# Kernel tuning notes

Hardware: AMD Instinct MI355X
Metric: run time of the kernel (lower is better)

Reference implementation:

```python
import jax, jax.numpy as jnp
import numpy as np

BN_EPS = 1e-5

def _bn(x, g, b):
    # BatchNorm1d, training-mode batch statistics
    mu = x.mean(axis=0)
    var = x.var(axis=0)
    return g * (x - mu) / jnp.sqrt(var + BN_EPS) + b

def setup_inputs() -> dict:
    key = jax.random.key(0)
    ks = jax.random.split(key, 10)
    B2, D_in, D1, DIMS, C = 16384, 1024, 512, 256, 40
    B = B2 // 2
    def w(k, shape, fan_in):
        return jax.random.normal(k, shape, jnp.float32) / np.float32(np.sqrt(fan_in))
    return {
        "lufeat": jax.random.normal(ks[0], (B2, D_in), jnp.float32),
        "llabel": jax.random.randint(ks[1], (B,), 0, C),
        "W1": w(ks[2], (D_in, D1), D_in), "b1": jnp.zeros(D1, jnp.float32),
        "W2": w(ks[3], (D1, DIMS), D1), "b2": jnp.zeros(DIMS, jnp.float32),
        "W3": w(ks[4], (DIMS + C, 256), DIMS + C), "b3": jnp.zeros(256, jnp.float32),
        "W4": w(ks[5], (256, 64), 256), "b4": jnp.zeros(64, jnp.float32),
        "W5": w(ks[6], (64, 1), 64), "b5": jnp.zeros(1, jnp.float32),
        "g1": jnp.ones(256, jnp.float32), "be1": jnp.zeros(256, jnp.float32),
        "g2": jnp.ones(64, jnp.float32), "be2": jnp.zeros(64, jnp.float32),
        "mbank0": jax.random.normal(ks[7], (C, DIMS), jnp.float32),
        "start0": jnp.zeros(C, jnp.float32),
    }

def reference(lufeat, llabel, W1, b1, W2, b2, W3, b3, W4, b4, W5, b5,
              g1, be1, g2, be2, mbank0, start0):
    B = lufeat.shape[0] // 2
    h = (lufeat @ W1 + b1) @ W2 + b2            # [2B, dims]
    h = h / jnp.linalg.norm(h, axis=1, keepdims=True)
    lfeat, ufeat = h[:B], h[B:]

    # Sequential per-sample memory-bank scatter/EMA update (detached feats)
    lf_sg = jax.lax.stop_gradient(lfeat)
    def step(carry, xs):
        start, mbank = carry
        lab, feat = xs
        row = jnp.where(start[lab] == 0, feat, 0.9 * mbank[lab] + 0.1 * feat)
        return (start.at[lab].set(1.0), mbank.at[lab].set(row)), None
    (_, mbank), _ = jax.lax.scan(step, (start0, mbank0), (llabel, lf_sg))
    mbank = jax.lax.stop_gradient(mbank)

    # cdist retrieval: [B, C] euclidean distances
    lm = jnp.linalg.norm(lfeat[:, None, :] - mbank[None, :, :], axis=-1)
    lscores = lm.min(axis=-1)
    um = jnp.linalg.norm(ufeat[:, None, :] - mbank[None, :, :], axis=-1)

    uf = jnp.concatenate([ufeat, um], axis=-1)   # [B, dims + C]
    u = jax.nn.relu(_bn(uf @ W3 + b3, g1, be1))
    u = jax.nn.relu(_bn(u @ W4 + b4, g2, be2))   # dropout = identity (eval)
    uscores = u @ W5 + b5                        # [B, 1]
    return lscores, uscores, mbank
```

## Files before the change

### kernel.cpp

```cpp
#include <hip/hip_runtime.h>
#include <hip/hip_bf16.h>
#include <stdint.h>

typedef __attribute__((ext_vector_type(4))) float f32x4;
typedef __attribute__((ext_vector_type(8))) short s16x8;
typedef __attribute__((ext_vector_type(4))) unsigned short u16x4;
typedef __attribute__((ext_vector_type(4))) int i32x4;

#define B2T 16384
#define BH 8192
#define DIN 1024
#define DD1 512
#define DIMS 256
#define NC 40
#define CAPS 2048

__device__ __forceinline__ unsigned short f2b(float f) {
  unsigned int u = __builtin_bit_cast(unsigned int, f);
  u += 0x7FFFu + ((u >> 16) & 1u);
  return (unsigned short)(u >> 16);
}

__device__ __forceinline__ float b2f(unsigned short u) {
  return __builtin_bit_cast(float, ((unsigned int)u) << 16);
}

__device__ __forceinline__ void gload16(const void* g, void* l) {
  __builtin_amdgcn_global_load_lds(
      (const __attribute__((address_space(1))) void*)g,
      (__attribute__((address_space(3))) void*)l, 16, 0, 0);
}

__global__ __launch_bounds__(256) void prep_all(const float* __restrict__ lufeat,
                                                unsigned short* __restrict__ lufeatH,
                                                const float* __restrict__ W1,
                                                const float* __restrict__ W2,
                                                const float* __restrict__ b1,
                                                const float* __restrict__ b2,
                                                const float* __restrict__ W3,
                                                const float* __restrict__ W4,
                                                unsigned short* __restrict__ WeffT,
                                                float* __restrict__ beff,
                                                unsigned short* __restrict__ W3T,
                                                unsigned short* __restrict__ W4T,
                                                float* __restrict__ statz) {
  __shared__ float W1s[32][36];
  __shared__ float W2sT[32][36];
  int b = blockIdx.x, t = threadIdx.x;
  if (b < 1024) {
#pragma unroll
    for (int i = 0; i < 8; ++i) {
      int idx = b * 16384 + i * 2048 + t * 8;
      f32x4 v0 = *(const f32x4*)(lufeat + idx);
      f32x4 v1 = *(const f32x4*)(lufeat + idx + 4);
      s16x8 p;
      p[0] = (short)f2b(v0[0]); p[1] = (short)f2b(v0[1]);
      p[2] = (short)f2b(v0[2]); p[3] = (short)f2b(v0[3]);
      p[4] = (short)f2b(v1[0]); p[5] = (short)f2b(v1[1]);
      p[6] = (short)f2b(v1[2]); p[7] = (short)f2b(v1[3]);
      *(s16x8*)(lufeatH + idx) = p;
    }
  } else if (b < 1280) {
    int bb = b - 1024;
    int k0 = (bb & 31) * 32, n0 = (bb >> 5) * 32;
    int nn = t & 31, kq = t >> 5;
    f32x4 acc = (f32x4){0.f, 0.f, 0.f, 0.f};
    for (int j0 = 0; j0 < DD1; j0 += 32) {
#pragma unroll
      for (int i = 0; i < 4; ++i) {
        int idx = t + 256 * i;
        int kk = idx >> 5, jj = idx & 31;
        W1s[kk][jj] = W1[(size_t)(k0 + kk) * DD1 + j0 + jj];
        W2sT[jj][kk] = W2[(size_t)(j0 + kk) * DIMS + n0 + jj];
      }
      __syncthreads();
#pragma unroll
      for (int jj4 = 0; jj4 < 8; ++jj4) {
        f32x4 w2 = *(const f32x4*)&W2sT[nn][jj4 * 4];
        f32x4 w1_0 = *(const f32x4*)&W1s[kq * 4 + 0][jj4 * 4];
        f32x4 w1_1 = *(const f32x4*)&W1s[kq * 4 + 1][jj4 * 4];
        f32x4 w1_2 = *(const f32x4*)&W1s[kq * 4 + 2][jj4 * 4];
        f32x4 w1_3 = *(const f32x4*)&W1s[kq * 4 + 3][jj4 * 4];
        acc[0] += w1_0[0] * w2[0] + w1_0[1] * w2[1] + w1_0[2] * w2[2] + w1_0[3] * w2[3];
        acc[1] += w1_1[0] * w2[0] + w1_1[1] * w2[1] + w1_1[2] * w2[2] + w1_1[3] * w2[3];
        acc[2] += w1_2[0] * w2[0] + w1_2[1] * w2[1] + w1_2[2] * w2[2] + w1_2[3] * w2[3];
        acc[3] += w1_3[0] * w2[0] + w1_3[1] * w2[1] + w1_3[2] * w2[2] + w1_3[3] * w2[3];
      }
      __syncthreads();
    }
    u16x4 pk = {f2b(acc[0]), f2b(acc[1]), f2b(acc[2]), f2b(acc[3])};
    *(u16x4*)(WeffT + (size_t)(n0 + nn) * DIN + k0 + kq * 4) = pk;
  } else if (b == 1280) {
    float a0 = 0.f, a1 = 0.f, a2 = 0.f, a3 = 0.f, a4 = 0.f, a5 = 0.f, a6 = 0.f, a7 = 0.f;
    for (int j = 0; j < DD1; j += 8) {
      a0 += b1[j + 0] * W2[(size_t)(j + 0) * DIMS + t];
      a1 += b1[j + 1] * W2[(size_t)(j + 1) * DIMS + t];
      a2 += b1[j + 2] * W2[(size_t)(j + 2) * DIMS + t];
      a3 += b1[j + 3] * W2[(size_t)(j + 3) * DIMS + t];
      a4 += b1[j + 4] * W2[(size_t)(j + 4) * DIMS + t];
      a5 += b1[j + 5] * W2[(size_t)(j + 5) * DIMS + t];
      a6 += b1[j + 6] * W2[(size_t)(j + 6) * DIMS + t];
      a7 += b1[j + 7] * W2[(size_t)(j + 7) * DIMS + t];
    }
    beff[t] = b2[t] + (((a0 + a1) + (a2 + a3)) + ((a4 + a5) + (a6 + a7)));
  } else if (b < 1601) {
    int idx = (b - 1281) * 256 + t;
    int n = idx / 320, k = idx - n * 320;
    float v = (k < 296) ? W3[(size_t)k * 256 + n] : 0.0f;
    W3T[(size_t)n * 320 + k] = f2b(v);
  } else if (b < 1665) {
    int idx = (b - 1601) * 256 + t;
    int n = idx >> 8, k = idx & 255;
    W4T[(size_t)n * 256 + k] = f2b(W4[(size_t)k * 64 + n]);
  } else {
    for (int i = t; i < 680; i += 256) statz[i] = 0.0f;
  }
}

__global__ __launch_bounds__(256) void gemm1_dma(
    const unsigned short* __restrict__ AH, const unsigned short* __restrict__ BT,
    const float* __restrict__ bias, float* __restrict__ C,
    unsigned short* __restrict__ uf) {
  __shared__ __align__(16) char A_s[2][4096];
  __shared__ __align__(16) char B_s[2][32768];
  __shared__ float rs[4][32];
  int t = threadIdx.x, m0 = blockIdx.x * 32;
  int w = t >> 6, lane = t & 63, q = lane >> 4, ln = lane & 15;
  f32x4 acc[2][4];
#pragma unroll
  for (int mi = 0; mi < 2; ++mi)
#pragma unroll
    for (int ni = 0; ni < 4; ++ni) acc[mi][ni] = (f32x4){0.f, 0.f, 0.f, 0.f};

  auto dma = [&](int s, int bufi) {
    int kb = s * 64;
    {
      int row = t >> 3, j = t & 7;
      gload16(AH + (size_t)(m0 + row) * 1024 + kb + ((j ^ (row & 7)) * 8),
              A_s[bufi] + t * 16);
    }
#pragma unroll
    for (int i = 0; i < 8; ++i) {
      int ch = t + 256 * i, n = ch >> 3, j = ch & 7;
      gload16(BT + (size_t)n * 1024 + kb + ((j ^ (n & 7)) * 8),
              B_s[bufi] + (w * 64 + 256 * i) * 16);
    }
  };

  auto compute = [&](int bufi) {
#pragma unroll
    for (int k32 = 0; k32 < 64; k32 += 32) {
      int koff = (k32 + q * 8) * 2;
      s16x8 af[2];
#pragma unroll
      for (int mi = 0; mi < 2; ++mi) {
        int row = mi * 16 + ln;
        af[mi] = *(const s16x8*)(A_s[bufi] + ((row * 128 + koff) ^ ((row & 7) << 4)));
      }
      int nb0 = w * 64;
#pragma unroll
      for (int ni = 0; ni < 4; ++ni) {
        int brow = nb0 + ni * 16 + ln;
        s16x8 bfr = *(const s16x8*)(B_s[bufi] + ((brow * 128 + koff) ^ ((brow & 7) << 4)));
#pragma unroll
        for (int mi = 0; mi < 2; ++mi)
          acc[mi][ni] = __builtin_amdgcn_mfma_f32_16x16x32_bf16(af[mi], bfr, acc[mi][ni], 0, 0, 0);
      }
    }
  };

  dma(0, 0);
  __syncthreads();
  for (int s = 0; s < 16; ++s) {
    if (s + 1 < 16) dma(s + 1, (s + 1) & 1);
    compute(s & 1);
    __syncthreads();
  }

  float v[2][4][4];
#pragma unroll
  for (int mi = 0; mi < 2; ++mi)
#pragma unroll
    for (int ni = 0; ni < 4; ++ni) {
      float bv = bias[w * 64 + ni * 16 + ln];
#pragma unroll
      for (int r = 0; r < 4; ++r) v[mi][ni][r] = acc[mi][ni][r] + bv;
    }
  float p[2][4];
#pragma unroll
  for (int mi = 0; mi < 2; ++mi)
#pragma unroll
    for (int r = 0; r < 4; ++r) {
      float s = v[mi][0][r] * v[mi][0][r] + v[mi][1][r] * v[mi][1][r] +
                v[mi][2][r] * v[mi][2][r] + v[mi][3][r] * v[mi][3][r];
      s += __shfl_xor(s, 1); s += __shfl_xor(s, 2);
      s += __shfl_xor(s, 4); s += __shfl_xor(s, 8);
      p[mi][r] = s;
    }
  if (ln == 0) {
#pragma unroll
    for (int mi = 0; mi < 2; ++mi)
#pragma unroll
      for (int r = 0; r < 4; ++r) rs[w][mi * 16 + q * 4 + r] = p[mi][r];
  }
  __syncthreads();
  if (t < 32) {
    float s = rs[0][t] + rs[1][t] + rs[2][t] + rs[3][t];
    rs[0][t] = rsqrtf(s);
  }
  __syncthreads();
#pragma unroll
  for (int mi = 0; mi < 2; ++mi)
#pragma unroll
    for (int r = 0; r < 4; ++r) {
      int ribf = mi * 16 + q * 4 + r;
      float inv = rs[0][ribf];
      int grow = m0 + ribf;
#pragma unroll
      for (int ni = 0; ni < 4; ++ni) {
        int col = w * 64 + ni * 16 + ln;
        float nv = v[mi][ni][r] * inv;
        if (grow < BH)
          C[(size_t)grow * DIMS + col] = nv;
        else
          uf[(size_t)(grow - BH) * 320 + col] = f2b(nv);
      }
    }
}

template <int AMODE, int NB, int MI, int CW, int EPI, int K, int TPB>
__global__ __launch_bounds__(TPB) void gemm_core(
    const void* __restrict__ Aptr, int lda, const unsigned short* __restrict__ BT,
    const float* __restrict__ bias, float* __restrict__ C, int ldc,
    float* __restrict__ sums, float* __restrict__ ssqs,
    const float* __restrict__ bnsum, const float* __restrict__ bnssq,
    const float* __restrict__ bng, const float* __restrict__ bnbe,
    unsigned short* __restrict__ uf) {
  constexpr int NW = TPB / 64;
  constexpr int RG = NW / CW;
  constexpr int AR = RG * MI * 16;
  constexpr int ACH = AR * 8;
  constexpr int ABN = (ACH + TPB - 1) / TPB;
  constexpr int BBN = NB * 8 / TPB;
  constexpr int BBUF = NB * 128;
  constexpr int ALOADS = (AMODE == 1) ? ABN : 2 * ABN;
  constexpr bool UNIF = (ACH >= TPB);
  __shared__ __align__(16) short A_s[2][AR][72];
  __shared__ __align__(16) char B_s[2 * BBUF];
  __shared__ float rs[CW][AR];
  __shared__ float bsc_s[(AMODE == 2) ? 256 : 1];
  __shared__ float bsh_s[(AMODE == 2) ? 256 : 1];
  int t = threadIdx.x;
  int m0 = blockIdx.x * AR;
  int w = t >> 6, lane = t & 63, q = lane >> 4, ln = lane & 15;
  f32x4 acc[MI][4];
#pragma unroll
  for (int mi = 0; mi < MI; ++mi)
#pragma unroll
    for (int ni = 0; ni < 4; ++ni) acc[mi][ni] = (f32x4){0.f, 0.f, 0.f, 0.f};

  f32x4 pa0[ABN][2], pa1[ABN][2];
  s16x8 pab0[ABN], pab1[ABN];

  auto issue = [&](int kbase, f32x4 (&paX)[ABN][2], s16x8 (&pabX)[ABN]) {
    if (ACH >= TPB || t < ACH) {
#pragma unroll
      for (int i = 0; i < ABN; ++i) {
        int ch = t + TPB * i, row = ch >> 3, kp = (ch & 7) * 8;
        if constexpr (AMODE == 1) {
          const unsigned short* A = (const unsigned short*)Aptr;
          pabX[i] = *(const s16x8*)(A + (size_t)(m0 + row) * lda + kbase + kp);
        } else {
          const float* A = (const float*)Aptr;
          const f32x4* src = (const f32x4*)(A + (size_t)(m0 + row) * lda + kbase + kp);
          paX[i][0] = src[0];
          paX[i][1] = src[1];
        }
      }
    }
  };

  auto gloadB = [&](int kbase, int bufi) {
#pragma unroll
    for (int i = 0; i < BBN; ++i) {
      int ch = t + TPB * i;
      int n = ch >> 3, j = ch & 7;
      int ksw = (j ^ (n & 7)) * 8;
      gload16(BT + (size_t)n * K + kbase + ksw,
              B_s + bufi * BBUF + (w * 64 + TPB * i) * 16);
    }
  };

  auto stage = [&](int kk, int bufi, f32x4 (&paX)[ABN][2], s16x8 (&pabX)[ABN]) {
    if (ACH >= TPB || t < ACH) {
#pragma unroll
      for (int i = 0; i < ABN; ++i) {
        int ch = t + TPB * i, row = ch >> 3, kp = (ch & 7) * 8;
        if constexpr (AMODE == 1) {
          *(s16x8*)&A_s[bufi][row][kp] = pabX[i];
        } else {
          f32x4 v0 = paX[i][0], v1 = paX[i][1];
          if constexpr (AMODE == 2) {
            float vv[8] = {v0[0], v0[1], v0[2], v0[3], v1[0], v1[1], v1[2], v1[3]};
#pragma unroll
            for (int j = 0; j < 8; ++j) {
              int f = kk + kp + j;
              vv[j] = fmaxf(vv[j] * bsc_s[f] + bsh_s[f], 0.0f);
            }
            v0 = (f32x4){vv[0], vv[1], vv[2], vv[3]};
            v1 = (f32x4){vv[4], vv[5], vv[6], vv[7]};
          }
          s16x8 p;
          p[0] = (short)f2b(v0[0]); p[1] = (short)f2b(v0[1]);
          p[2] = (short)f2b(v0[2]); p[3] = (short)f2b(v0[3]);
          p[4] = (short)f2b(v1[0]); p[5] = (short)f2b(v1[1]);
          p[6] = (short)f2b(v1[2]); p[7] = (short)f2b(v1[3]);
          *(s16x8*)&A_s[bufi][row][kp] = p;
        }
      }
    }
  };

  auto compute = [&](int cur) {
#pragma unroll
    for (int k32 = 0; k32 < 64; k32 += 32) {
      s16x8 af[MI];
      int ab = (w / CW) * MI * 16;
#pragma unroll
      for (int mi = 0; mi < MI; ++mi)
        af[mi] = *(const s16x8*)&A_s[cur][ab + mi * 16 + ln][k32 + q * 8];
      int nb0 = (w % CW) * 64;
#pragma unroll
      for (int ni = 0; ni < 4; ++ni) {
        int brow = nb0 + ni * 16 + ln;
        int bb = (brow * 128 + (k32 + q * 8) * 2) ^ ((brow & 7) << 4);
        s16x8 bfr = *(const s16x8*)(B_s + cur * BBUF + bb);
#pragma unroll
        for (int mi = 0; mi < MI; ++mi)
          acc[mi][ni] = __builtin_amdgcn_mfma_f32_16x16x32_bf16(af[mi], bfr, acc[mi][ni], 0, 0, 0);
      }
    }
  };

  auto kbar = [&](bool keepA) {
    if constexpr (UNIF) {
      if (keepA)
        asm volatile("s_waitcnt vmcnt(%0) lgkmcnt(0)" ::"n"(ALOADS) : "memory");
      else
        asm volatile("s_waitcnt vmcnt(0) lgkmcnt(0)" ::: "memory");
      __builtin_amdgcn_s_barrier();
      __builtin_amdgcn_sched_barrier(0);
    } else {
      __syncthreads();
    }
  };

  if constexpr (AMODE == 2) {
    if (t < 256) {
      float mu = bnsum[t] * (1.0f / 8192.0f);
      float var = bnssq[t] * (1.0f / 8192.0f) - mu * mu;
      float sc = bng[t] * rsqrtf(var + 1e-5f);
      bsc_s[t] = sc;
      bsh_s[t] = bnbe[t] - mu * sc;
    }
    __syncthreads();
  }

  const int nst = K >> 6;
  issue(0, pa0, pab0);
  gloadB(0, 0);
  __builtin_amdgcn_sched_barrier(0);
  if (nst > 1) issue(64, pa1, pab1);
  stage(0, 0, pa0, pab0);
  kbar(nst > 1);

  for (int s = 0; s < nst; s += 2) {
    if (s + 1 < nst) gloadB((s + 1) << 6, 1);
    __builtin_amdgcn_sched_barrier(0);
    if (s + 2 < nst) issue((s + 2) << 6, pa0, pab0);
    compute(0);
    if (s + 1 < nst) stage((s + 1) << 6, 1, pa1, pab1);
    kbar(s + 2 < nst);
    if (s + 1 < nst) {
      if (s + 2 < nst) gloadB((s + 2) << 6, 0);
      __builtin_amdgcn_sched_barrier(0);
      if (s + 3 < nst) issue((s + 3) << 6, pa1, pab1);
      compute(1);
      if (s + 2 < nst) stage((s + 2) << 6, 0, pa0, pab0);
      kbar(s + 3 < nst);
    }
  }

  float v[MI][4][4];
#pragma unroll
  for (int mi = 0; mi < MI; ++mi)
#pragma unroll
    for (int ni = 0; ni < 4; ++ni) {
      float bv = bias[(w % CW) * 64 + ni * 16 + ln];
#pragma unroll
      for (int r = 0; r < 4; ++r) v[mi][ni][r] = acc[mi][ni][r] + bv;
    }

#pragma unroll
  for (int mi = 0; mi < MI; ++mi)
#pragma unroll
    for (int ni = 0; ni < 4; ++ni)
#pragma unroll
      for (int r = 0; r < 4; ++r) {
        int grow = m0 + (w / CW) * MI * 16 + mi * 16 + q * 4 + r;
        int col = (w % CW) * 64 + ni * 16 + ln;
        C[(size_t)grow * ldc + col] = v[mi][ni][r];
      }
  if constexpr (EPI == 2 || EPI == 3) {
#pragma unroll
    for (int ni = 0; ni < 4; ++ni) {
      float s = 0.f, s2 = 0.f;
#pragma unroll
      for (int mi = 0; mi < MI; ++mi)
#pragma unroll
        for (int r = 0; r < 4; ++r) {
          float x = v[mi][ni][r];
          s += x; s2 += x * x;
        }
      s += __shfl_xor(s, 16); s += __shfl_xor(s, 32);
      s2 += __shfl_xor(s2, 16); s2 += __shfl_xor(s2, 32);
      if (q == 0) {
        int col = (w % CW) * 64 + ni * 16 + ln;
        atomicAdd(&sums[col], s);
        atomicAdd(&ssqs[col], s2);
      }
    }
  }
}

__global__ __launch_bounds__(256) void bank_kernel(const int* __restrict__ llabel,
                                                   const float* __restrict__ Hn,
                                                   const float* __restrict__ mbank0,
                                                   const float* __restrict__ start0,
                                                   float* __restrict__ mbank_out,
                                                   float* __restrict__ msq) {
  __shared__ i32x4 lab4[BH / 4];
  __shared__ int idx_s[CAPS];
  __shared__ float redp[256];
  __shared__ int wcnt[4];
  int t = threadIdx.x, c = blockIdx.x >> 2, dq = blockIdx.x & 3;
  int w = t >> 6, lane = t & 63;
  const float l09 = -0.15200309344504997f;

  for (int i = t; i < BH / 4; i += 256) lab4[i] = ((const i32x4*)llabel)[i];
  __syncthreads();
  const int* lab_s = (const int*)lab4;

  int base0 = w * (BH / 4);
  int cnt = 0;
  for (int b = 0; b < BH / 4; b += 64)
    cnt += (int)__popcll(__ballot(lab_s[base0 + b + lane] == c));
  if (lane == 0) wcnt[w] = cnt;
  __syncthreads();
  int off = 0;
#pragma unroll
  for (int i = 0; i < 4; ++i)
    if (i < w) off += wcnt[i];
  int Ktot = wcnt[0] + wcnt[1] + wcnt[2] + wcnt[3];
  int running = off;
  for (int b = 0; b < BH / 4; b += 64) {
    bool hit = lab_s[base0 + b + lane] == c;
    unsigned long long mk = __ballot(hit);
    if (hit) {
      int pos = running + (int)__popcll(mk & ((1ull << lane) - 1ull));
      if (pos < CAPS) idx_s[pos] = base0 + b + lane;
    }
    running += (int)__popcll(mk);
  }
  __syncthreads();
  int K = Ktot < CAPS ? Ktot : CAPS;
  bool fresh = (start0[c] == 0.0f);
  int dcol = t & 63, rr = t >> 6;
  int d = dq * 64 + dcol;
  float p0 = 0.f, p1 = 0.f, p2 = 0.f, p3 = 0.f;
  if (K > 0) {
    float w0fold = fresh ? exp2f((float)K * l09) : 0.f;
    int m = rr;
    for (; m + 12 < K; m += 16) {
      float e = (float)(K - 1 - m);
      float wa = 0.1f * exp2f(e * l09) + (m == 0 ? w0fold : 0.f);
      p0 += wa * Hn[(size_t)idx_s[m] * DIMS + d];
      p1 += 0.1f * exp2f((e - 4.f) * l09) * Hn[(size_t)idx_s[m + 4] * DIMS + d];
      p2 += 0.1f * exp2f((e - 8.f) * l09) * Hn[(size_t)idx_s[m + 8] * DIMS + d];
      p3 += 0.1f * exp2f((e - 12.f) * l09) * Hn[(size_t)idx_s[m + 12] * DIMS + d];
    }
    for (; m < K; m += 4) {
      float wa = 0.1f * exp2f((float)(K - 1 - m) * l09) + (m == 0 ? w0fold : 0.f);
      p0 += wa * Hn[(size_t)idx_s[m] * DIMS + d];
    }
  }
  redp[rr * 64 + dcol] = (p0 + p1) + (p2 + p3);
  __syncthreads();
  if (t < 64) {
    int dd = dq * 64 + t;
    float out;
    if (K == 0) {
      out = mbank0[(size_t)c * DIMS + dd];
    } else {
      float base_v = fresh ? 0.f : exp2f((float)K * l09) * mbank0[(size_t)c * DIMS + dd];
      out = ((redp[t] + redp[64 + t]) + (redp[128 + t] + redp[192 + t])) + base_v;
    }
    mbank_out[(size_t)c * DIMS + dd] = out;
    float vv = out * out;
#pragma unroll
    for (int o = 32; o; o >>= 1) vv += __shfl_xor(vv, o);
    if (t == 0) atomicAdd(&msq[c], vv);
  }
}

__global__ __launch_bounds__(256) void dist_kernel(const float* __restrict__ Hn,
                                                   const float* __restrict__ mbank,
                                                   const float* __restrict__ msq,
                                                   float* __restrict__ lscores,
                                                   unsigned short* __restrict__ uf) {
  __shared__ float Ms[NC][260];
  __shared__ float Hs[32][260];
  __shared__ float msq_s[NC];
  int t = threadIdx.x;
  int r0 = blockIdx.x * 32;
  for (int e = t; e < NC * 64; e += 256) {
    int i = e >> 6, d0 = (e & 63) * 4;
    *(f32x4*)&Ms[i][d0] = *(const f32x4*)(mbank + (size_t)i * DIMS + d0);
  }
  if (r0 < BH) {
    for (int e = t; e < 32 * 64; e += 256) {
      int i = e >> 6, d0 = (e & 63) * 4;
      *(f32x4*)&Hs[i][d0] = *(const f32x4*)(Hn + (size_t)(r0 + i) * DIMS + d0);
    }
  } else {
    for (int e = t; e < 32 * 32; e += 256) {
      int i = e >> 5, d0 = (e & 31) * 8;
      s16x8 vb = *(const s16x8*)(uf + (size_t)(r0 - BH + i) * 320 + d0);
#pragma unroll
      for (int j = 0; j < 8; ++j) Hs[i][d0 + j] = b2f((unsigned short)vb[j]);
    }
  }
  if (t < NC) msq_s[t] = msq[t];
  __syncthreads();
  int r = t >> 3, c0 = (t & 7) * 5;
  float g0 = 0, g1 = 0, g2 = 0, g3 = 0, g4 = 0;
  for (int d = 0; d < DIMS; d += 4) {
    f32x4 f = *(const f32x4*)&Hs[r][d];
    f32x4 m0v = *(const f32x4*)&Ms[c0 + 0][d];
    f32x4 m1v = *(const f32x4*)&Ms[c0 + 1][d];
    f32x4 m2v = *(const f32x4*)&Ms[c0 + 2][d];
    f32x4 m3v = *(const f32x4*)&Ms[c0 + 3][d];
    f32x4 m4v = *(const f32x4*)&Ms[c0 + 4][d];
    g0 += f[0] * m0v[0] + f[1] * m0v[1] + f[2] * m0v[2] + f[3] * m0v[3];
    g1 += f[0] * m1v[0] + f[1] * m1v[1] + f[2] * m1v[2] + f[3] * m1v[3];
    g2 += f[0] * m2v[0] + f[1] * m2v[1] + f[2] * m2v[2] + f[3] * m2v[3];
    g3 += f[0] * m3v[0] + f[1] * m3v[1] + f[2] * m3v[2] + f[3] * m3v[3];
    g4 += f[0] * m4v[0] + f[1] * m4v[1] + f[2] * m4v[2] + f[3] * m4v[3];
  }
  int row = r0 + r;
  float d2[5];
  d2[0] = 1.0f + msq_s[c0 + 0] - 2.0f * g0;
  d2[1] = 1.0f + msq_s[c0 + 1] - 2.0f * g1;
  d2[2] = 1.0f + msq_s[c0 + 2] - 2.0f * g2;
  d2[3] = 1.0f + msq_s[c0 + 3] - 2.0f * g3;
  d2[4] = 1.0f + msq_s[c0 + 4] - 2.0f * g4;
  if (row < BH) {
    float mn = fminf(fminf(fminf(d2[0], d2[1]), fminf(d2[2], d2[3])), d2[4]);
    mn = fminf(mn, __shfl_xor(mn, 1, 8));
    mn = fminf(mn, __shfl_xor(mn, 2, 8));
    mn = fminf(mn, __shfl_xor(mn, 4, 8));
    if ((t & 7) == 0) lscores[row] = sqrtf(fmaxf(mn, 0.0f));
  } else {
    unsigned short* dst = uf + (size_t)(row - BH) * 320 + 256 + c0;
#pragma unroll
    for (int qq = 0; qq < 5; ++qq) dst[qq] = f2b(sqrtf(fmaxf(d2[qq], 0.0f)));
  }
}

__global__ __launch_bounds__(256) void uscore_bn(const float* __restrict__ y2,
                                                 const float* __restrict__ sums2,
                                                 const float* __restrict__ ssqs2,
                                                 const float* __restrict__ g2,
                                                 const float* __restrict__ be2,
                                                 const float* __restrict__ W5,
                                                 const float* __restrict__ b5,
                                                 float* __restrict__ out) {
  int t = threadIdx.x;
  int wv = t >> 6, lane = t & 63;
  int row = blockIdx.x * 4 + wv;
  float mu = sums2[lane] * (1.0f / 8192.0f);
  float var = ssqs2[lane] * (1.0f / 8192.0f) - mu * mu;
  float sc = g2[lane] * rsqrtf(var + 1e-5f);
  float sh = be2[lane] - mu * sc;
  float v = fmaxf(y2[(size_t)row * 64 + lane] * sc + sh, 0.0f) * W5[lane];
#pragma unroll
  for (int o = 32; o; o >>= 1) v += __shfl_xor(v, o);
  if (lane == 0) out[row] = v + b5[0];
}

extern "C" void kernel_launch(void* const* d_in, const int* in_sizes, int n_in,
                              void* d_out, int out_size, void* d_ws, size_t ws_size,
                              hipStream_t stream) {
  const float* lufeat = (const float*)d_in[0];
  const int* llabel = (const int*)d_in[1];
  const float* W1 = (const float*)d_in[2];
  const float* b1 = (const float*)d_in[3];
  const float* W2 = (const float*)d_in[4];
  const float* b2 = (const float*)d_in[5];
  const float* W3 = (const float*)d_in[6];
  const float* b3 = (const float*)d_in[7];
  const float* W4 = (const float*)d_in[8];
  const float* b4 = (const float*)d_in[9];
  const float* W5 = (const float*)d_in[10];
  const float* b5 = (const float*)d_in[11];
  const float* g1 = (const float*)d_in[12];
  const float* be1 = (const float*)d_in[13];
  const float* g2 = (const float*)d_in[14];
  const float* be2 = (const float*)d_in[15];
  const float* mbank0 = (const float*)d_in[16];
  const float* start0 = (const float*)d_in[17];

  char* ws = (char*)d_ws;
  unsigned short* WeffT = (unsigned short*)(ws + 0);
  float* Hraw = (float*)(ws + 524288);
  float* ybuf = (float*)(ws + 524288);
  float* y2 = (float*)(ws + 8912896);
  unsigned short* uf = (unsigned short*)(ws + 17301504);
  unsigned short* W3T = (unsigned short*)(ws + 22544384);
  unsigned short* W4T = (unsigned short*)(ws + 22708224);
  float* beff = (float*)(ws + 22740992);
  float* sums1 = (float*)(ws + 22742016);
  float* ssq1 = sums1 + 256;
  float* sums2 = ssq1 + 256;
  float* ssq2 = sums2 + 64;
  float* msq = (float*)(ws + 22744576);
  unsigned short* lufeatH = (unsigned short*)(ws + 25165824);

  float* lscores = (float*)d_out;
  float* uscores = lscores + 8192;
  float* mbank = uscores + 8192;

  prep_all<<<1666, 256, 0, stream>>>(lufeat, lufeatH, W1, W2, b1, b2, W3, W4,
                                     WeffT, beff, W3T, W4T, sums1);
  gemm1_dma<<<512, 256, 0, stream>>>(lufeatH, WeffT, beff, Hraw, uf);
  bank_kernel<<<160, 256, 0, stream>>>(llabel, Hraw, mbank0, start0, mbank, msq);
  dist_kernel<<<512, 256, 0, stream>>>(Hraw, mbank, msq, lscores, uf);
  gemm_core<1, 256, 1, 4, 2, 320, 512><<<256, 512, 0, stream>>>(
      uf, 320, W3T, b3, ybuf, 256,
      sums1, ssq1, nullptr, nullptr, nullptr, nullptr, nullptr);
  gemm_core<2, 64, 1, 1, 3, 256, 256><<<128, 256, 0, stream>>>(
      ybuf, 256, W4T, b4, y2, 64,
      sums2, ssq2, sums1, ssq1, g1, be1, nullptr);
  uscore_bn<<<2048, 256, 0, stream>>>(y2, sums2, ssq2, g2, be2, W5, b5, uscores);
}
```

Baseline: 238.2 us.

## Split input bf16 conversion into own kernel and add DMA-based W3 GEMM

Moves the fp32-to-bf16 conversion of lufeat out of the fused prep kernel into a separate launch with 2048 blocks, shrinking prep_all to the weight preprocessing. Replaces the templated gemm_core for the W3 layer with a dedicated gemm2_dma kernel that uses global_load_lds direct-to-LDS loads, XOR-swizzled layout, double buffering and 16-row tiles across 512 blocks, with BN statistics accumulated via atomics. This is meant to raise parallelism and cut register-staged loads, at the cost of an extra launch and more atomic traffic. The unused rs shared array is dropped from gemm_core.

```diff
diff --git a/kernel.cpp b/kernel.cpp
--- a/kernel.cpp
+++ b/kernel.cpp
@@ -31,9 +31,24 @@
       (__attribute__((address_space(3))) void*)l, 16, 0, 0);
 }
 
-__global__ __launch_bounds__(256) void prep_all(const float* __restrict__ lufeat,
-                                                unsigned short* __restrict__ lufeatH,
-                                                const float* __restrict__ W1,
+__global__ __launch_bounds__(256) void hcvt(const float* __restrict__ in,
+                                            unsigned short* __restrict__ out) {
+  size_t base = (size_t)blockIdx.x * 8192 + (size_t)threadIdx.x * 8;
+#pragma unroll
+  for (int i = 0; i < 4; ++i) {
+    size_t idx = base + (size_t)i * 2048;
+    f32x4 v0 = *(const f32x4*)(in + idx);
+    f32x4 v1 = *(const f32x4*)(in + idx + 4);
+    s16x8 p;
+    p[0] = (short)f2b(v0[0]); p[1] = (short)f2b(v0[1]);
+    p[2] = (short)f2b(v0[2]); p[3] = (short)f2b(v0[3]);
+    p[4] = (short)f2b(v1[0]); p[5] = (short)f2b(v1[1]);
+    p[6] = (short)f2b(v1[2]); p[7] = (short)f2b(v1[3]);
+    *(s16x8*)(out + idx) = p;
+  }
+}
+
+__global__ __launch_bounds__(256) void prep_all(const float* __restrict__ W1,
                                                 const float* __restrict__ W2,
                                                 const float* __restrict__ b1,
                                                 const float* __restrict__ b2,
@@ -47,22 +62,8 @@
   __shared__ float W1s[32][36];
   __shared__ float W2sT[32][36];
   int b = blockIdx.x, t = threadIdx.x;
-  if (b < 1024) {
-#pragma unroll
-    for (int i = 0; i < 8; ++i) {
-      int idx = b * 16384 + i * 2048 + t * 8;
-      f32x4 v0 = *(const f32x4*)(lufeat + idx);
-      f32x4 v1 = *(const f32x4*)(lufeat + idx + 4);
-      s16x8 p;
-      p[0] = (short)f2b(v0[0]); p[1] = (short)f2b(v0[1]);
-      p[2] = (short)f2b(v0[2]); p[3] = (short)f2b(v0[3]);
-      p[4] = (short)f2b(v1[0]); p[5] = (short)f2b(v1[1]);
-      p[6] = (short)f2b(v1[2]); p[7] = (short)f2b(v1[3]);
-      *(s16x8*)(lufeatH + idx) = p;
-    }
-  } else if (b < 1280) {
-    int bb = b - 1024;
-    int k0 = (bb & 31) * 32, n0 = (bb >> 5) * 32;
+  if (b < 256) {
+    int k0 = (b & 31) * 32, n0 = (b >> 5) * 32;
     int nn = t & 31, kq = t >> 5;
     f32x4 acc = (f32x4){0.f, 0.f, 0.f, 0.f};
     for (int j0 = 0; j0 < DD1; j0 += 32) {
@@ -90,7 +91,7 @@
     }
     u16x4 pk = {f2b(acc[0]), f2b(acc[1]), f2b(acc[2]), f2b(acc[3])};
     *(u16x4*)(WeffT + (size_t)(n0 + nn) * DIN + k0 + kq * 4) = pk;
-  } else if (b == 1280) {
+  } else if (b == 256) {
     float a0 = 0.f, a1 = 0.f, a2 = 0.f, a3 = 0.f, a4 = 0.f, a5 = 0.f, a6 = 0.f, a7 = 0.f;
     for (int j = 0; j < DD1; j += 8) {
       a0 += b1[j + 0] * W2[(size_t)(j + 0) * DIMS + t];
@@ -103,13 +104,13 @@
       a7 += b1[j + 7] * W2[(size_t)(j + 7) * DIMS + t];
     }
     beff[t] = b2[t] + (((a0 + a1) + (a2 + a3)) + ((a4 + a5) + (a6 + a7)));
-  } else if (b < 1601) {
-    int idx = (b - 1281) * 256 + t;
+  } else if (b < 577) {
+    int idx = (b - 257) * 256 + t;
     int n = idx / 320, k = idx - n * 320;
     float v = (k < 296) ? W3[(size_t)k * 256 + n] : 0.0f;
     W3T[(size_t)n * 320 + k] = f2b(v);
-  } else if (b < 1665) {
-    int idx = (b - 1601) * 256 + t;
+  } else if (b < 641) {
+    int idx = (b - 577) * 256 + t;
     int n = idx >> 8, k = idx & 255;
     W4T[(size_t)n * 256 + k] = f2b(W4[(size_t)k * 64 + n]);
   } else {
@@ -226,6 +227,77 @@
           uf[(size_t)(grow - BH) * 320 + col] = f2b(nv);
       }
     }
+}
+
+__global__ __launch_bounds__(256) void gemm2_dma(
+    const unsigned short* __restrict__ AH, const unsigned short* __restrict__ BT,
+    const float* __restrict__ bias, float* __restrict__ C,
+    float* __restrict__ sums, float* __restrict__ ssqs) {
+  __shared__ __align__(16) char A_s[2][2048];
+  __shared__ __align__(16) char B_s[2][32768];
+  int t = threadIdx.x, m0 = blockIdx.x * 16;
+  int w = t >> 6, lane = t & 63, q = lane >> 4, ln = lane & 15;
+  f32x4 acc[4];
+#pragma unroll
+  for (int ni = 0; ni < 4; ++ni) acc[ni] = (f32x4){0.f, 0.f, 0.f, 0.f};
+
+  auto dma = [&](int s, int bufi) {
+    int kb = s * 64;
+    if (t < 128) {
+      int row = t >> 3, j = t & 7;
+      gload16(AH + (size_t)(m0 + row) * 320 + kb + ((j ^ (row & 7)) * 8),
+              A_s[bufi] + t * 16);
+    }
+#pragma unroll
+    for (int i = 0; i < 8; ++i) {
+      int ch = t + 256 * i, n = ch >> 3, j = ch & 7;
+      gload16(BT + (size_t)n * 320 + kb + ((j ^ (n & 7)) * 8),
+              B_s[bufi] + (w * 64 + 256 * i) * 16);
+    }
+  };
+
+  auto compute = [&](int bufi) {
+#pragma unroll
+    for (int k32 = 0; k32 < 64; k32 += 32) {
+      int koff = (k32 + q * 8) * 2;
+      int arow = ln;
+      s16x8 af = *(const s16x8*)(A_s[bufi] + ((arow * 128 + koff) ^ ((arow & 7) << 4)));
+      int nb0 = w * 64;
+#pragma unroll
+      for (int ni = 0; ni < 4; ++ni) {
+        int brow = nb0 + ni * 16 + ln;
+        s16x8 bfr = *(const s16x8*)(B_s[bufi] + ((brow * 128 + koff) ^ ((brow & 7) << 4)));
+        acc[ni] = __builtin_amdgcn_mfma_f32_16x16x32_bf16(af, bfr, acc[ni], 0, 0, 0);
+      }
+    }
+  };
+
+  dma(0, 0);
+  __syncthreads();
+  for (int s = 0; s < 5; ++s) {
+    if (s + 1 < 5) dma(s + 1, (s + 1) & 1);
+    compute(s & 1);
+    __syncthreads();
+  }
+
+#pragma unroll
+  for (int ni = 0; ni < 4; ++ni) {
+    int col = w * 64 + ni * 16 + ln;
+    float bv = bias[col];
+    float s = 0.f, s2 = 0.f;
+#pragma unroll
+    for (int r = 0; r < 4; ++r) {
+      float x = acc[ni][r] + bv;
+      C[(size_t)(m0 + q * 4 + r) * 256 + col] = x;
+      s += x; s2 += x * x;
+    }
+    s += __shfl_xor(s, 16); s += __shfl_xor(s, 32);
+    s2 += __shfl_xor(s2, 16); s2 += __shfl_xor(s2, 32);
+    if (q == 0) {
+      atomicAdd(&sums[col], s);
+      atomicAdd(&ssqs[col], s2);
+    }
+  }
 }
 
 template <int AMODE, int NB, int MI, int CW, int EPI, int K, int TPB>
@@ -247,7 +319,6 @@
   constexpr bool UNIF = (ACH >= TPB);
   __shared__ __align__(16) short A_s[2][AR][72];
   __shared__ __align__(16) char B_s[2 * BBUF];
-  __shared__ float rs[CW][AR];
   __shared__ float bsc_s[(AMODE == 2) ? 256 : 1];
   __shared__ float bsh_s[(AMODE == 2) ? 256 : 1];
   int t = threadIdx.x;
@@ -640,14 +711,12 @@
   float* uscores = lscores + 8192;
   float* mbank = uscores + 8192;
 
-  prep_all<<<1666, 256, 0, stream>>>(lufeat, lufeatH, W1, W2, b1, b2, W3, W4,
-                                     WeffT, beff, W3T, W4T, sums1);
+  hcvt<<<2048, 256, 0, stream>>>(lufeat, lufeatH);
+  prep_all<<<642, 256, 0, stream>>>(W1, W2, b1, b2, W3, W4, WeffT, beff, W3T, W4T, sums1);
   gemm1_dma<<<512, 256, 0, stream>>>(lufeatH, WeffT, beff, Hraw, uf);
   bank_kernel<<<160, 256, 0, stream>>>(llabel, Hraw, mbank0, start0, mbank, msq);
   dist_kernel<<<512, 256, 0, stream>>>(Hraw, mbank, msq, lscores, uf);
-  gemm_core<1, 256, 1, 4, 2, 320, 512><<<256, 512, 0, stream>>>(
-      uf, 320, W3T, b3, ybuf, 256,
-      sums1, ssq1, nullptr, nullptr, nullptr, nullptr, nullptr);
+  gemm2_dma<<<512, 256, 0, stream>>>(uf, W3T, b3, ybuf, sums1, ssq1);
   gemm_core<2, 64, 1, 1, 3, 256, 256><<<128, 256, 0, stream>>>(
       ybuf, 256, W4T, b4, y2, 64,
       sums2, ssq2, sums1, ssq1, g1, be1, nullptr);
```

New measurement: 242.6 us. Within noise of the previous version (+1.8%).
